# Optimization experiments

Hardware: AMD Instinct MI355X
Metric: run time of the kernel (lower is better)

The kernel has to match this reference:

```python
import jax, jax.numpy as jnp
import numpy as np

B, S, D = 4, 4096, 2048
H, HD = 16, 128
FFN = 8192
CAP = 0.25
TOP_K = int(S * CAP)  # 1024
EPS = 1e-6


def rmsnorm(x, g):
    return x * jax.lax.rsqrt(jnp.mean(x * x, axis=-1, keepdims=True) + EPS) * g


def apply_rope(x, cos, sin):
    # x: [b,t,h,hd]; cos/sin: [t, hd//2]
    half = x.shape[-1] // 2
    x1, x2 = x[..., :half], x[..., half:]
    c = cos[None, :, None, :]
    s = sin[None, :, None, :]
    return jnp.concatenate([x1 * c - x2 * s, x1 * s + x2 * c], axis=-1)


def transformer_block(x, mask, freqs_cis, g1, wq, wk, wv, wo, g2, w1, w3, w2):
    b, t, d = x.shape
    cos, sin = freqs_cis[..., 0], freqs_cis[..., 1]
    h = rmsnorm(x, g1)
    q = (h @ wq).reshape(b, t, H, HD)
    k = (h @ wk).reshape(b, t, H, HD)
    v = (h @ wv).reshape(b, t, H, HD)
    q = apply_rope(q, cos, sin)
    k = apply_rope(k, cos, sin)
    scores = jnp.einsum('bqhd,bkhd->bhqk', q, k) / np.sqrt(HD) + mask[None, None]
    attn = jax.nn.softmax(scores, axis=-1)
    o = jnp.einsum('bhqk,bkhd->bqhd', attn, v).reshape(b, t, d) @ wo
    x = x + o
    h2 = rmsnorm(x, g2)
    x = x + (jax.nn.silu(h2 @ w1) * (h2 @ w3)) @ w2
    return x, None


def setup_inputs() -> dict:
    key = jax.random.key(0)
    ks = jax.random.split(key, 12)
    w = lambda k, shp: jax.random.normal(k, shp, dtype=jnp.float32) * 0.02
    return {
        'x': jax.random.normal(ks[0], (B, S, D), dtype=jnp.float32),
        'mask': jnp.zeros((TOP_K, TOP_K), dtype=jnp.float32),
        'freqs_cis': jax.random.uniform(ks[1], (TOP_K, HD // 2, 2), dtype=jnp.float32),
        'w_router': w(ks[2], (D,)),
        'g1': jnp.ones((D,), dtype=jnp.float32),
        'wq': w(ks[3], (D, D)),
        'wk': w(ks[4], (D, D)),
        'wv': w(ks[5], (D, D)),
        'wo': w(ks[6], (D, D)),
        'g2': jnp.ones((D,), dtype=jnp.float32),
        'w1': w(ks[7], (D, FFN)),
        'w3': w(ks[8], (D, FFN)),
        'w2': w(ks[9], (FFN, D)),
    }


def reference(x, mask, freqs_cis, w_router, g1, wq, wk, wv, wo, g2, w1, w3, w2):
    b, s, d = x.shape
    # router: Linear(dim, 1, bias=False) -> [b, s]
    router_logits = jnp.einsum('bsd,d->bs', x, w_router)
    vals, idx = jax.lax.top_k(router_logits, TOP_K)  # [b, k]
    # sort selected indices ascending; permute weights to match (softmax is
    # permutation-equivariant so softmax-then-permute == torch's gather order)
    order = jnp.argsort(idx, axis=1)
    sel = jnp.take_along_axis(idx, order, axis=1)          # [b, k]
    w_sel = jnp.take_along_axis(vals, order, axis=1)       # [b, k]
    r_weights = jax.nn.softmax(w_sel, axis=1)[..., None]   # [b, k, 1]
    filtered_x = jnp.take_along_axis(x, sel[..., None], axis=1)  # [b, k, d]
    x_out, _ = transformer_block(filtered_x, mask, freqs_cis, g1, wq, wk, wv, wo, g2, w1, w3, w2)
    xw_out = r_weights * x_out
    b_idx = jnp.arange(b)[:, None]
    out = x.at[b_idx, sel].add(xw_out)
    return out
```

## Files before the change

### kernel.cpp

```cpp
#include <hip/hip_runtime.h>
#include <cstdint>
#include <cstddef>

#define NB 4
#define NS 4096
#define ND 2048
#define NH 16
#define NHD 128
#define NT 1024
#define NF 8192

typedef __bf16 bf16;
typedef __bf16 bf16x8 __attribute__((ext_vector_type(8)));
typedef __bf16 bf16x4 __attribute__((ext_vector_type(4)));
typedef float  f32x4  __attribute__((ext_vector_type(4)));

typedef const __attribute__((address_space(1))) void* gptr_t;
typedef __attribute__((address_space(3))) void* lptr_t;

__device__ __forceinline__ float wave_sum(float v) {
#pragma unroll
    for (int off = 32; off > 0; off >>= 1) v += __shfl_xor(v, off);
    return v;
}
__device__ __forceinline__ float wave_max(float v) {
#pragma unroll
    for (int off = 32; off > 0; off >>= 1) v = fmaxf(v, __shfl_xor(v, off));
    return v;
}

__global__ __launch_bounds__(256) void router_k(const float* __restrict__ x,
                                                const float* __restrict__ wr,
                                                float* __restrict__ logits) {
    __shared__ float r4[4];
    long long row = blockIdx.x;
    const float4* xr = (const float4*)(x + row * ND);
    const float4* w4 = (const float4*)wr;
    float p = 0.f;
    for (int i = threadIdx.x; i < ND / 4; i += 256) {
        float4 a = xr[i], b = w4[i];
        p += a.x * b.x + a.y * b.y + a.z * b.z + a.w * b.w;
    }
    p = wave_sum(p);
    if ((threadIdx.x & 63) == 0) r4[threadIdx.x >> 6] = p;
    __syncthreads();
    if (threadIdx.x == 0) logits[row] = r4[0] + r4[1] + r4[2] + r4[3];
}

__global__ __launch_bounds__(1024) void topk_k(const float* __restrict__ logits,
                                               int* __restrict__ sel,
                                               float* __restrict__ rw) {
    __shared__ unsigned long long keys[NS];
    __shared__ float r16[16];
    __shared__ float bmax, bsum;
    const int bb = blockIdx.x;
    const int tid = threadIdx.x;
    const float* lg = logits + (long long)bb * NS;

    for (int i = tid; i < NS; i += 1024) {
        unsigned u = __float_as_uint(lg[i]);
        u = (u & 0x80000000u) ? ~u : (u | 0x80000000u);
        keys[i] = ((unsigned long long)u << 32) | (unsigned)(NS - 1 - i);
    }
    __syncthreads();
    for (int k = 2; k <= NS; k <<= 1) {
        for (int j = k >> 1; j > 0; j >>= 1) {
            for (int i = tid; i < NS; i += 1024) {
                int ixj = i ^ j;
                if (ixj > i) {
                    unsigned long long a = keys[i], c = keys[ixj];
                    bool up = ((i & k) == 0);
                    if (up ? (a < c) : (a > c)) { keys[i] = c; keys[ixj] = a; }
                }
            }
            __syncthreads();
        }
    }
    unsigned long long a0 = keys[tid];
    __syncthreads();
    {
        unsigned idx_ = NS - 1 - (unsigned)(a0 & 0xFFFFFFFFu);
        unsigned uval = (unsigned)(a0 >> 32);
        keys[tid] = ((unsigned long long)idx_ << 32) | uval;
    }
    __syncthreads();
    for (int k = 2; k <= NT; k <<= 1) {
        for (int j = k >> 1; j > 0; j >>= 1) {
            int i = tid, ixj = i ^ j;
            if (i < NT && ixj > i) {
                unsigned long long a = keys[i], c = keys[ixj];
                bool up = ((i & k) == 0);
                if (up ? (a > c) : (a < c)) { keys[i] = c; keys[ixj] = a; }
            }
            __syncthreads();
        }
    }
    unsigned long long kk = keys[tid];
    int si = (int)(kk >> 32);
    unsigned u = (unsigned)(kk & 0xFFFFFFFFu);
    u = (u & 0x80000000u) ? (u ^ 0x80000000u) : ~u;
    float val = __uint_as_float(u);

    const int wid = tid >> 6, lane = tid & 63;
    float mx = wave_max(val);
    if (lane == 0) r16[wid] = mx;
    __syncthreads();
    if (tid == 0) {
        float m = r16[0];
        for (int i = 1; i < 16; i++) m = fmaxf(m, r16[i]);
        bmax = m;
    }
    __syncthreads();
    float e = __expf(val - bmax);
    float s = wave_sum(e);
    if (lane == 0) r16[wid] = s;
    __syncthreads();
    if (tid == 0) {
        float t = 0.f;
        for (int i = 0; i < 16; i++) t += r16[i];
        bsum = t;
    }
    __syncthreads();
    sel[bb * NT + tid] = si;
    rw[bb * NT + tid] = e / bsum;
}

__global__ __launch_bounds__(256) void gather_k(const float* __restrict__ x,
                                                const int* __restrict__ sel,
                                                float* __restrict__ xf) {
    int gid = blockIdx.x * 256 + threadIdx.x;
    int col = gid & (ND / 4 - 1);
    int row = gid >> 9;
    int bb = row >> 10;
    int s = sel[row];
    ((float4*)xf)[gid] = ((const float4*)x)[((long long)bb * NS + s) * (ND / 4) + col];
}

__global__ __launch_bounds__(256) void rmsnorm_k(const float* __restrict__ x,
                                                 const float* __restrict__ g,
                                                 bf16* __restrict__ out) {
    __shared__ float r4[4];
    __shared__ float scl;
    long long row = blockIdx.x;
    const float4* xr = (const float4*)(x + row * ND);
    int i0 = threadIdx.x, i1 = threadIdx.x + 256;
    float4 a = xr[i0], b = xr[i1];
    float ss = a.x * a.x + a.y * a.y + a.z * a.z + a.w * a.w +
               b.x * b.x + b.y * b.y + b.z * b.z + b.w * b.w;
    ss = wave_sum(ss);
    if ((threadIdx.x & 63) == 0) r4[threadIdx.x >> 6] = ss;
    __syncthreads();
    if (threadIdx.x == 0)
        scl = rsqrtf((r4[0] + r4[1] + r4[2] + r4[3]) * (1.0f / ND) + 1e-6f);
    __syncthreads();
    float s = scl;
    const float4* g4 = (const float4*)g;
    float4 ga = g4[i0], gb = g4[i1];
    bf16x4 o0, o1;
    o0[0] = (bf16)(a.x * s * ga.x); o0[1] = (bf16)(a.y * s * ga.y);
    o0[2] = (bf16)(a.z * s * ga.z); o0[3] = (bf16)(a.w * s * ga.w);
    o1[0] = (bf16)(b.x * s * gb.x); o1[1] = (bf16)(b.y * s * gb.y);
    o1[2] = (bf16)(b.z * s * gb.z); o1[3] = (bf16)(b.w * s * gb.w);
    *(bf16x4*)(out + row * ND + i0 * 4) = o0;
    *(bf16x4*)(out + row * ND + i1 * 4) = o1;
}

__global__ __launch_bounds__(256) void transpose_to_bf16(const float* __restrict__ in,
                                                         bf16* __restrict__ out,
                                                         int R, int C) {
    __shared__ float tile[32][33];
    int bx = blockIdx.x * 32;
    int by = blockIdx.y * 32;
    int tx = threadIdx.x & 31;
    int ty = threadIdx.x >> 5;
#pragma unroll
    for (int i = 0; i < 4; i++)
        tile[ty + 8 * i][tx] = in[(long long)(by + ty + 8 * i) * C + bx + tx];
    __syncthreads();
#pragma unroll
    for (int i = 0; i < 4; i++)
        out[(long long)(bx + ty + 8 * i) * R + by + tx] = (bf16)tile[tx][ty + 8 * i];
}

__global__ __launch_bounds__(256) void transpose4_nd(const float* __restrict__ s0,
                                                     const float* __restrict__ s1,
                                                     const float* __restrict__ s2,
                                                     const float* __restrict__ s3,
                                                     bf16* __restrict__ d_wqkv,
                                                     bf16* __restrict__ d_wo) {
    __shared__ float tile[32][33];
    const int z = blockIdx.z;
    const float* in = (z == 0) ? s0 : (z == 1) ? s1 : (z == 2) ? s2 : s3;
    bf16* out = (z < 3) ? (d_wqkv + (size_t)z * ND * ND) : d_wo;
    int bx = blockIdx.x * 32;
    int by = blockIdx.y * 32;
    int tx = threadIdx.x & 31;
    int ty = threadIdx.x >> 5;
#pragma unroll
    for (int i = 0; i < 4; i++)
        tile[ty + 8 * i][tx] = in[(long long)(by + ty + 8 * i) * ND + bx + tx];
    __syncthreads();
#pragma unroll
    for (int i = 0; i < 4; i++)
        out[(long long)(bx + ty + 8 * i) * ND + by + tx] = (bf16)tile[tx][ty + 8 * i];
}

__global__ __launch_bounds__(256) void transpose2_ff(const float* __restrict__ s0,
                                                     const float* __restrict__ s1,
                                                     bf16* __restrict__ dst) {
    __shared__ float tile[32][33];
    const int z = blockIdx.z;
    const float* in = z ? s1 : s0;
    bf16* out = dst + (size_t)z * ND * NF;
    int bx = blockIdx.x * 32;
    int by = blockIdx.y * 32;
    int tx = threadIdx.x & 31;
    int ty = threadIdx.x >> 5;
#pragma unroll
    for (int i = 0; i < 4; i++)
        tile[ty + 8 * i][tx] = in[(long long)(by + ty + 8 * i) * NF + bx + tx];
    __syncthreads();
#pragma unroll
    for (int i = 0; i < 4; i++)
        out[(long long)(bx + ty + 8 * i) * ND + by + tx] = (bf16)tile[tx][ty + 8 * i];
}

__global__ __launch_bounds__(256) void rope_qk_k(const bf16* __restrict__ QKV,
                                                 const float* __restrict__ fr,
                                                 bf16* __restrict__ Q,
                                                 bf16* __restrict__ K) {
    int gid = blockIdx.x * 256 + threadIdx.x;
    int hd = gid & 63;
    int h = (gid >> 6) & 15;
    int t = (gid >> 10) & (NT - 1);
    int bb = gid >> 20;
    float c = fr[t * 128 + hd * 2 + 0];
    float s = fr[t * 128 + hd * 2 + 1];
    long long base = ((long long)bb * NT + t) * (3 * ND) + h * NHD;
    float q1 = (float)QKV[base + hd],      q2 = (float)QKV[base + hd + 64];
    float k1 = (float)QKV[base + ND + hd], k2 = (float)QKV[base + ND + hd + 64];
    long long ob = (((long long)(bb * NH + h)) * NT + t) * NHD;
    Q[ob + hd]      = (bf16)(q1 * c - q2 * s);
    Q[ob + hd + 64] = (bf16)(q1 * s + q2 * c);
    K[ob + hd]      = (bf16)(k1 * c - k2 * s);
    K[ob + hd + 64] = (bf16)(k1 * s + k2 * c);
}

__global__ __launch_bounds__(256) void vtr_k(const bf16* __restrict__ QKV,
                                             bf16* __restrict__ Vt) {
    __shared__ bf16 tile[64][136];
    const int tt = blockIdx.x * 64;
    const int bh = blockIdx.y;
    const int bb = bh >> 4, h = bh & 15;
    const int tid = threadIdx.x;

    const int lt = tid >> 4;
    const int ld = (tid & 15) * 8;
#pragma unroll
    for (int i = 0; i < 4; i++) {
        int t = i * 16 + lt;
        bf16x8 v = *(const bf16x8*)(QKV + ((size_t)(bb * NT) + tt + t) * (3 * ND)
                                    + 2 * ND + h * NHD + ld);
        *(bf16x8*)&tile[t][ld] = v;
    }
    __syncthreads();

    const int d = tid >> 1;
    const int j0 = (tid & 1) * 32;
    bf16 tmp[32];
#pragma unroll
    for (int j = 0; j < 32; j++) tmp[j] = tile[j0 + j][d];
    bf16* dst = Vt + ((size_t)bh * NHD + d) * NT + tt + j0;
#pragma unroll
    for (int j = 0; j < 4; j++)
        *(bf16x8*)(dst + j * 8) = *(const bf16x8*)(tmp + j * 8);
}

__global__ __launch_bounds__(256) void copy_k(const float4* __restrict__ in,
                                              float4* __restrict__ out, long long n) {
    for (long long i = (long long)blockIdx.x * 256 + threadIdx.x; i < n;
         i += (long long)gridDim.x * 256)
        out[i] = in[i];
}

__global__ __launch_bounds__(256, 2) void flash_k(
    const bf16* __restrict__ Qr,
    const bf16* __restrict__ Kr,
    const bf16* __restrict__ Vt,
    bf16* __restrict__ O) {
    __shared__ char lds[81920];

    const int tid = threadIdx.x;
    const int lane = tid & 63;
    const int w = tid >> 6;
    const int lm = lane & 15, lq = lane >> 4;
    const int lm7 = lm & 7;

    const int bh = blockIdx.y;
    const int q0 = blockIdx.x * 128;
    const bf16* Qb = Qr + (size_t)bh * NT * NHD;
    const bf16* Kb = Kr + (size_t)bh * NT * NHD;
    const bf16* Vb = Vt + (size_t)bh * NHD * NT;

    const int krow = tid >> 4;
    const int kc_s = (tid & 15);
    const int vrow = tid >> 3;
    const int vc_s = (tid & 7);

    bf16x8 q[2][4];
#pragma unroll
    for (int mi = 0; mi < 2; mi++)
#pragma unroll
        for (int ks = 0; ks < 4; ks++)
            q[mi][ks] = *(const bf16x8*)(Qb + (size_t)(q0 + w * 32 + mi * 16 + lm) * NHD
                                         + lq * 8 + ks * 32);

    f32x4 o0[8], o1[8];
#pragma unroll
    for (int i = 0; i < 8; i++) {
        f32x4 zz = {0.f, 0.f, 0.f, 0.f};
        o0[i] = zz; o1[i] = zz;
    }
    float m0[4], m1[4], l0[4], l1[4];
#pragma unroll
    for (int r = 0; r < 4; r++) {
        m0[r] = -3.0e38f; m1[r] = -3.0e38f; l0[r] = 0.f; l1[r] = 0.f;
    }

    char* Pb = lds + 65536 + w * 4096;
    const float kscal = 0.08838834764831845f * 1.4426950408889634f;

#pragma unroll
    for (int i = 0; i < 4; i++) {
        int row = i * 16 + krow;
        __builtin_amdgcn_global_load_lds(
            (gptr_t)(Kb + (size_t)row * NHD + (kc_s ^ (row & 7)) * 8),
            (lptr_t)(lds + i * 4096 + tid * 16), 16, 0, 0);
    }
#pragma unroll
    for (int i = 0; i < 4; i++) {
        int row = i * 32 + vrow;
        __builtin_amdgcn_global_load_lds(
            (gptr_t)(Vb + (size_t)row * NT + (vc_s ^ (row & 7)) * 8),
            (lptr_t)(lds + 32768 + i * 4096 + tid * 16), 16, 0, 0);
    }
    __syncthreads();

    for (int c = 0; c < 16; ++c) {
        char* Kl = lds + (c & 1) * 16384;
        char* Vl = lds + 32768 + (c & 1) * 16384;

        if (c < 15) {
            const int key1 = (c + 1) * 64;
            char* Kd = lds + ((c + 1) & 1) * 16384;
            char* Vd = lds + 32768 + ((c + 1) & 1) * 16384;
#pragma unroll
            for (int i = 0; i < 4; i++) {
                int row = i * 16 + krow;
                __builtin_amdgcn_global_load_lds(
                    (gptr_t)(Kb + (size_t)(key1 + row) * NHD + (kc_s ^ (row & 7)) * 8),
                    (lptr_t)(Kd + i * 4096 + tid * 16), 16, 0, 0);
            }
#pragma unroll
            for (int i = 0; i < 4; i++) {
                int row = i * 32 + vrow;
                __builtin_amdgcn_global_load_lds(
                    (gptr_t)(Vb + (size_t)row * NT + key1 + (vc_s ^ (row & 7)) * 8),
                    (lptr_t)(Vd + i * 4096 + tid * 16), 16, 0, 0);
            }
        }

        f32x4 s0[4], s1[4];
#pragma unroll
        for (int ni = 0; ni < 4; ni++) {
            f32x4 zz = {0.f, 0.f, 0.f, 0.f};
            s0[ni] = zz; s1[ni] = zz;
        }
        __builtin_amdgcn_s_setprio(1);
#pragma unroll
        for (int ni = 0; ni < 4; ni++) {
#pragma unroll
            for (int ks = 0; ks < 4; ks++) {
                bf16x8 kf = *(const bf16x8*)(Kl + (lm + 16 * ni) * 256
                                             + (((lq + 4 * ks) ^ lm7) << 4));
                s0[ni] = __builtin_amdgcn_mfma_f32_16x16x32_bf16(q[0][ks], kf, s0[ni], 0, 0, 0);
                s1[ni] = __builtin_amdgcn_mfma_f32_16x16x32_bf16(q[1][ks], kf, s1[ni], 0, 0, 0);
            }
        }
        __builtin_amdgcn_s_setprio(0);

#pragma unroll
        for (int ni = 0; ni < 4; ni++)
#pragma unroll
            for (int r = 0; r < 4; r++) {
                s0[ni][r] *= kscal;
                s1[ni][r] *= kscal;
            }

        float sc0[4], sc1[4];
#pragma unroll
        for (int r = 0; r < 4; r++) {
            float a0 = fmaxf(fmaxf(s0[0][r], s0[1][r]), fmaxf(s0[2][r], s0[3][r]));
            float a1 = fmaxf(fmaxf(s1[0][r], s1[1][r]), fmaxf(s1[2][r], s1[3][r]));
#pragma unroll
            for (int o = 1; o < 16; o <<= 1) {
                a0 = fmaxf(a0, __shfl_xor(a0, o));
                a1 = fmaxf(a1, __shfl_xor(a1, o));
            }
            float mn0 = fmaxf(m0[r], a0);
            float mn1 = fmaxf(m1[r], a1);
            sc0[r] = exp2f(m0[r] - mn0);
            sc1[r] = exp2f(m1[r] - mn1);
            m0[r] = mn0; m1[r] = mn1;

            float rs0 = 0.f, rs1 = 0.f;
#pragma unroll
            for (int ni = 0; ni < 4; ni++) {
                float p0 = exp2f(s0[ni][r] - mn0);
                float p1 = exp2f(s1[ni][r] - mn1);
                s0[ni][r] = p0; s1[ni][r] = p1;
                rs0 += p0; rs1 += p1;
            }
#pragma unroll
            for (int o = 1; o < 16; o <<= 1) {
                rs0 += __shfl_xor(rs0, o);
                rs1 += __shfl_xor(rs1, o);
            }
            l0[r] = l0[r] * sc0[r] + rs0;
            l1[r] = l1[r] * sc1[r] + rs1;
        }
#pragma unroll
        for (int ni = 0; ni < 8; ni++)
#pragma unroll
            for (int r = 0; r < 4; r++) {
                o0[ni][r] *= sc0[r];
                o1[ni][r] *= sc1[r];
            }

#pragma unroll
        for (int ni = 0; ni < 4; ni++)
#pragma unroll
            for (int r = 0; r < 4; r++) {
                int q_l0 = lq * 4 + r;
                int q_l1 = 16 + q_l0;
                int cw = (lm >> 3) + 2 * ni;
                *(bf16*)(Pb + q_l0 * 128 + ((cw ^ (q_l0 & 7)) << 4) + (lm7 << 1)) =
                    (bf16)s0[ni][r];
                *(bf16*)(Pb + q_l1 * 128 + ((cw ^ (q_l1 & 7)) << 4) + (lm7 << 1)) =
                    (bf16)s1[ni][r];
            }
        asm volatile("s_waitcnt lgkmcnt(0)" ::: "memory");
        __builtin_amdgcn_sched_barrier(0);

        __builtin_amdgcn_s_setprio(1);
#pragma unroll
        for (int ks = 0; ks < 2; ks++) {
            bf16x8 pa0 = *(const bf16x8*)(Pb + lm * 128 + (((lq + 4 * ks) ^ lm7) << 4));
            bf16x8 pa1 = *(const bf16x8*)(Pb + (lm + 16) * 128 + (((lq + 4 * ks) ^ lm7) << 4));
#pragma unroll
            for (int ni = 0; ni < 8; ni++) {
                bf16x8 vf = *(const bf16x8*)(Vl + (lm + 16 * ni) * 128
                                             + (((lq + 4 * ks) ^ lm7) << 4));
                o0[ni] = __builtin_amdgcn_mfma_f32_16x16x32_bf16(pa0, vf, o0[ni], 0, 0, 0);
                o1[ni] = __builtin_amdgcn_mfma_f32_16x16x32_bf16(pa1, vf, o1[ni], 0, 0, 0);
            }
        }
        __builtin_amdgcn_s_setprio(0);

        __syncthreads();
    }

    const int bb = bh >> 4, h = bh & 15;
    float rl0[4], rl1[4];
#pragma unroll
    for (int r = 0; r < 4; r++) { rl0[r] = 1.f / l0[r]; rl1[r] = 1.f / l1[r]; }
#pragma unroll
    for (int ni = 0; ni < 8; ni++) {
#pragma unroll
        for (int r = 0; r < 4; r++) {
            int col = h * 128 + lm + 16 * ni;
            long long r0 = (long long)bb * NT + q0 + w * 32 + lq * 4 + r;
            O[(r0) * ND + col]      = (bf16)(o0[ni][r] * rl0[r]);
            O[(r0 + 16) * ND + col] = (bf16)(o1[ni][r] * rl1[r]);
        }
    }
}

#define G256_SB() __builtin_amdgcn_sched_barrier(0)
#define G256_LGKM(n) do { asm volatile("s_waitcnt lgkmcnt(" #n ")" ::: "memory"); \
    __builtin_amdgcn_sched_barrier(0); } while (0)
#define G256_VMC(n) do { asm volatile("s_waitcnt vmcnt(" #n ")" ::: "memory"); \
    __builtin_amdgcn_sched_barrier(0); } while (0)

#define MFMA_Q(mlo, nlo) do { \
    __builtin_amdgcn_s_setprio(1); \
    _Pragma("unroll") \
    for (int _ks = 0; _ks < 2; _ks++) \
    _Pragma("unroll") \
    for (int _mi = 0; _mi < 4; _mi++) \
    _Pragma("unroll") \
    for (int _ni = 0; _ni < 2; _ni++) \
        acc[(mlo) + _mi][(nlo) + _ni] = __builtin_amdgcn_mfma_f32_16x16x32_bf16( \
            a[(mlo) + _mi][_ks], b[(nlo) + _ni][_ks], acc[(mlo) + _mi][(nlo) + _ni], \
            0, 0, 0); \
    __builtin_amdgcn_s_setprio(0); \
} while (0)

template <int MODE>
__global__ __launch_bounds__(512, 2) void gemm256(
    const bf16* __restrict__ A, int lda,
    const bf16* __restrict__ Bt, int ldb,
    void* __restrict__ Cv, int ldc,
    int K, float alpha,
    const bf16* __restrict__ Bt2,
    const float* __restrict__ res, const int* __restrict__ selp,
    const float* __restrict__ rwp, float* __restrict__ outp) {

    constexpr bool DUALB = (MODE == 6);
    constexpr bool N128  = (MODE == 2 || MODE == 5 || MODE == 7);
    constexpr bool NI4   = !N128;
    constexpr int  BBUF  = N128 ? 16384 : 32768;
    constexpr int  BUFS  = 32768 + BBUF;
    constexpr int  bStep2 = DUALB ? 16384 : 4096;
    __shared__ char smem[2 * BUFS];

    const int tid = threadIdx.x;
    const int lane = tid & 63;
    const int wid = tid >> 6;
    const int wm = N128 ? (wid >> 1) : (wid >> 2);
    const int wn = N128 ? (wid & 1) : (wid & 3);
    const int lm = lane & 15, lq = lane >> 4;

    const int nx = gridDim.x;
    const int orig = blockIdx.y * nx + blockIdx.x;
    const int xcd = orig & 7;
    const int r_ = orig >> 3;
    const int mi_ = r_ & 7, ni_ = r_ >> 3;
    const int nT = (DUALB || N128) ? 128 : 256;
    const int m0 = ((xcd >> 2) * 8 + mi_) * 256;
    const int n0 = ((xcd & 3) * (nx >> 2) + ni_) * nT;
    const long long kz = (long long)blockIdx.z * K;

    const int srow = tid >> 3;
    const int skc = ((tid & 7) ^ (srow & 7)) * 8;
    const long long stA = (long long)64 * lda;
    const long long stB = (long long)64 * ldb;
    const bf16* gA = A + (long long)(m0 + srow) * lda + kz + skc;
    const bf16* gB0 = Bt + (long long)(n0 + srow) * ldb + kz + skc;
    const bf16* gB2 = DUALB ? Bt2 + (long long)(n0 + srow) * ldb + kz + skc
                            : gB0 + 2 * stB;

    char* sm = (char*)smem;
    const int sdst = tid * 16;

    auto stage = [&](int c, int t) {
        char* lA = sm + c * BUFS + sdst;
        long long ko = (long long)t * 64;
#pragma unroll
        for (int i = 0; i < 4; i++)
            __builtin_amdgcn_global_load_lds((gptr_t)(gA + i * stA + ko),
                                             (lptr_t)(lA + i * 8192), 16, 0, 0);
        char* lB = sm + c * BUFS + 32768 + sdst;
        __builtin_amdgcn_global_load_lds((gptr_t)(gB0 + ko), (lptr_t)lB, 16, 0, 0);
        __builtin_amdgcn_global_load_lds((gptr_t)(gB0 + stB + ko),
                                         (lptr_t)(lB + 8192), 16, 0, 0);
        if constexpr (NI4) {
            __builtin_amdgcn_global_load_lds((gptr_t)(gB2 + ko),
                                             (lptr_t)(lB + 16384), 16, 0, 0);
            __builtin_amdgcn_global_load_lds((gptr_t)(gB2 + stB + ko),
                                             (lptr_t)(lB + 24576), 16, 0, 0);
        }
    };

    const int swz = (lq ^ (lm & 7)) << 4;
    const int aoff = ((N128 ? wm * 64 : wm * 128) + lm) * 128 + swz;
    const int boff = ((N128 ? wn * 64 : (DUALB ? wn * 32 : wn * 64)) + lm) * 128 + swz;

    f32x4 acc[8][4];
#pragma unroll
    for (int i = 0; i < 8; i++)
#pragma unroll
        for (int j = 0; j < 4; j++) {
            f32x4 zz = {0.f, 0.f, 0.f, 0.f};
            acc[i][j] = zz;
        }
    bf16x8 a[8][2], b[4][2];

    auto ldA4 = [&](char* bA, int lo) {
#pragma unroll
        for (int mi2 = 0; mi2 < 4; mi2++) {
            a[lo + mi2][0] = *(const bf16x8*)(bA + aoff + (lo + mi2) * 2048);
            a[lo + mi2][1] = *(const bf16x8*)(bA + (aoff ^ 64) + (lo + mi2) * 2048);
        }
    };
    auto ldB2 = [&](char* bB, int lo) {
#pragma unroll
        for (int ni2 = 0; ni2 < 2; ni2++) {
            int ix = lo + ni2;
            int o;
            if constexpr (N128)
                o = boff + ix * 2048;
            else
                o = boff + (ix & 1) * 2048 + (ix >> 1) * bStep2;
            b[ix][0] = *(const bf16x8*)(bB + o);
            b[ix][1] = *(const bf16x8*)(bB + (o ^ 64));
        }
    };

    const int NTk = K >> 6;

    stage(0, 0);
    stage(1, 1);
    if constexpr (NI4) { G256_VMC(8); } else { G256_VMC(6); }
    __builtin_amdgcn_s_barrier();
    G256_SB();

    for (int t = 0; t < NTk; ++t) {
        const int c = t & 1;
        char* bA = sm + c * BUFS;
        char* bB = bA + 32768;

        if constexpr (N128) {
            ldA4(bA, 0);
            ldB2(bB, 0);
            G256_SB();
            ldB2(bB, 2);
            G256_SB();

            G256_LGKM(4);
            MFMA_Q(0, 0);
            G256_LGKM(0);
            __builtin_amdgcn_s_barrier();
            G256_SB();
            const bool more = (t + 2 < NTk);
            if (more) stage(c, t + 2);
            G256_SB();
            MFMA_Q(0, 2);
            if (more) { G256_VMC(6); } else { G256_VMC(0); }
            __builtin_amdgcn_s_barrier();
            G256_SB();
        } else {
            ldA4(bA, 0);
            ldB2(bB, 0);
            G256_SB();
            ldB2(bB, 2);
            G256_SB();
            ldA4(bA, 4);
            G256_SB();

            G256_LGKM(12);
            MFMA_Q(0, 0);
            G256_LGKM(8);
            MFMA_Q(0, 2);
            G256_LGKM(0);
            __builtin_amdgcn_s_barrier();
            G256_SB();
            const bool more = (t + 2 < NTk);
            if (more) stage(c, t + 2);
            G256_SB();
            MFMA_Q(4, 0);
            MFMA_Q(4, 2);
            if (more) { G256_VMC(8); } else { G256_VMC(0); }
            __builtin_amdgcn_s_barrier();
            G256_SB();
        }
    }

    if constexpr (MODE == 6) {
        bf16* C = (bf16*)Cv;
#pragma unroll
        for (int mi = 0; mi < 8; mi++) {
#pragma unroll
            for (int ni = 0; ni < 2; ni++) {
                const int row = m0 + wm * 128 + mi * 16 + lq * 4;
                const int col = n0 + wn * 32 + ni * 16 + lm;
#pragma unroll
                for (int r = 0; r < 4; r++) {
                    float v1 = acc[mi][ni][r];
                    float v3 = acc[mi][ni + 2][r];
                    C[(long long)(row + r) * ldc + col] =
                        (bf16)((v1 / (1.f + __expf(-v1))) * v3);
                }
            }
        }
    } else {
#pragma unroll
        for (int mi = 0; mi < 4; mi++) {
#pragma unroll
            for (int ni = 0; ni < 4; ni++) {
                const int row = m0 + wm * 64 + mi * 16 + lq * 4;
                const int col = n0 + wn * 64 + ni * 16 + lm;
#pragma unroll
                for (int r = 0; r < 4; r++) {
                    float v = alpha * acc[mi][ni][r];
                    long long rr = row + r;
                    if constexpr (MODE == 7) {
                        bf16* C = (bf16*)Cv;
                        C[rr * ldc + col] = (bf16)v;
                    } else if constexpr (MODE == 2) {
                        float* C = (float*)Cv;
                        C[rr * ldc + col] += v;
                    } else {
                        int bb2 = (int)(rr >> 10);
                        int s = selp[rr];
                        float add = rwp[rr] * (v + res[rr * (long long)ND + col]);
                        outp[((long long)bb2 * NS + s) * ND + col] += add;
                    }
                }
            }
        }
    }
}

extern "C" void kernel_launch(void* const* d_in, const int* in_sizes, int n_in,
                              void* d_out, int out_size, void* d_ws, size_t ws_size,
                              hipStream_t stream) {
    const float* x  = (const float*)d_in[0];
    const float* fr = (const float*)d_in[2];
    const float* wr = (const float*)d_in[3];
    const float* g1 = (const float*)d_in[4];
    const float* wq = (const float*)d_in[5];
    const float* wk = (const float*)d_in[6];
    const float* wv = (const float*)d_in[7];
    const float* wo = (const float*)d_in[8];
    const float* g2 = (const float*)d_in[9];
    const float* w1 = (const float*)d_in[10];
    const float* w3 = (const float*)d_in[11];
    const float* w2 = (const float*)d_in[12];
    float* out = (float*)d_out;

    char* ws = (char*)d_ws;
    size_t off = 0;
    auto take = [&](size_t bytes) -> char* {
        char* p = ws + off;
        off += (bytes + 255) & ~(size_t)255;
        return p;
    };
    int*   sel    = (int*)take((size_t)NB * NT * 4);
    float* rw     = (float*)take((size_t)NB * NT * 4);
    float* logits = (float*)take((size_t)NB * NS * 4);
    float* xf     = (float*)take((size_t)NB * NT * ND * 4);
    bf16*  hbuf   = (bf16*)take((size_t)NB * NT * ND * 2);
    bf16*  wqkv_t = (bf16*)take((size_t)3 * ND * ND * 2);
    bf16*  wo_t   = (bf16*)take((size_t)ND * ND * 2);
    bf16*  Obuf   = (bf16*)take((size_t)NB * NT * ND * 2);
    char* xr = ws + off;
    bf16* QKV = (bf16*)xr;
    bf16* Qr  = QKV + (size_t)NB * NT * 3 * ND;
    bf16* Kr  = Qr + (size_t)NB * NT * ND;
    bf16* Vt  = Kr + (size_t)NB * NT * ND;
    bf16* w1_t  = (bf16*)xr;
    bf16* w3_t  = w1_t + (size_t)ND * NF;
    bf16* w2_t  = w3_t + (size_t)ND * NF;
    bf16* inter = w2_t + (size_t)ND * NF;

    router_k<<<NB * NS, 256, 0, stream>>>(x, wr, logits);
    topk_k<<<NB, 1024, 0, stream>>>(logits, sel, rw);
    gather_k<<<(NB * NT * ND / 4) / 256, 256, 0, stream>>>(x, sel, xf);
    rmsnorm_k<<<NB * NT, 256, 0, stream>>>(xf, g1, hbuf);

    transpose4_nd<<<dim3(ND / 32, ND / 32, 4), 256, 0, stream>>>(
        wq, wk, wv, wo, wqkv_t, wo_t);

    gemm256<7><<<dim3(3 * ND / 128, NB * NT / 256, 1), 512, 0, stream>>>(
        hbuf, ND, wqkv_t, ND, QKV, 3 * ND, ND, 1.0f,
        nullptr, nullptr, nullptr, nullptr, nullptr);

    rope_qk_k<<<(NB * NT * NH * 64) / 256, 256, 0, stream>>>(QKV, fr, Qr, Kr);
    vtr_k<<<dim3(NT / 64, NB * NH), 256, 0, stream>>>(QKV, Vt);

    flash_k<<<dim3(NT / 128, NB * NH), 256, 0, stream>>>(Qr, Kr, Vt, Obuf);

    gemm256<2><<<dim3(ND / 128, NB * NT / 256, 1), 512, 0, stream>>>(
        Obuf, ND, wo_t, ND, xf, ND, ND, 1.0f,
        nullptr, nullptr, nullptr, nullptr, nullptr);

    rmsnorm_k<<<NB * NT, 256, 0, stream>>>(xf, g2, hbuf);

    transpose2_ff<<<dim3(NF / 32, ND / 32, 2), 256, 0, stream>>>(w1, w3, w1_t);
    transpose_to_bf16<<<dim3(ND / 32, NF / 32), 256, 0, stream>>>(w2, w2_t, NF, ND);

    gemm256<6><<<dim3(NF / 128, NB * NT / 256, 1), 512, 0, stream>>>(
        hbuf, ND, w1_t, ND, inter, NF, ND, 1.0f,
        w3_t, nullptr, nullptr, nullptr, nullptr);

    copy_k<<<8192, 256, 0, stream>>>((const float4*)x, (float4*)out,
                                     (long long)NB * NS * ND / 4);
    gemm256<5><<<dim3(ND / 128, NB * NT / 256, 1), 512, 0, stream>>>(
        inter, NF, w2_t, NF, nullptr, ND, NF, 1.0f,
        nullptr, xf, sel, rw, out);
}
```

Before: 1.249 ms.

## Load B fragments directly from global into registers in dual-B GEMM

For the dual-weight (w1/w3) GEMM mode, B tiles are no longer staged through LDS. Each wave now loads its own B fragments straight from global memory into registers, prefetched one k-step ahead, while A stays double-buffered in LDS. The goal is to cut LDS traffic and shared-memory footprint so more blocks fit per CU. The trade-off is uncoalesced direct global loads, higher register pressure from the prefetch buffer, and loss of B reuse across waves. The non-N128 single-B path is removed, so only the dual-B and N128 modes remain supported.

```diff
diff --git a/kernel.cpp b/kernel.cpp
--- a/kernel.cpp
+++ b/kernel.cpp
@@ -518,10 +518,7 @@
 
     constexpr bool DUALB = (MODE == 6);
     constexpr bool N128  = (MODE == 2 || MODE == 5 || MODE == 7);
-    constexpr bool NI4   = !N128;
-    constexpr int  BBUF  = N128 ? 16384 : 32768;
-    constexpr int  BUFS  = 32768 + BBUF;
-    constexpr int  bStep2 = DUALB ? 16384 : 4096;
+    constexpr int  BUFS  = DUALB ? 32768 : 49152;
     __shared__ char smem[2 * BUFS];
 
     const int tid = threadIdx.x;
@@ -536,9 +533,8 @@
     const int xcd = orig & 7;
     const int r_ = orig >> 3;
     const int mi_ = r_ & 7, ni_ = r_ >> 3;
-    const int nT = (DUALB || N128) ? 128 : 256;
     const int m0 = ((xcd >> 2) * 8 + mi_) * 256;
-    const int n0 = ((xcd & 3) * (nx >> 2) + ni_) * nT;
+    const int n0 = ((xcd & 3) * (nx >> 2) + ni_) * 128;
     const long long kz = (long long)blockIdx.z * K;
 
     const int srow = tid >> 3;
@@ -547,34 +543,34 @@
     const long long stB = (long long)64 * ldb;
     const bf16* gA = A + (long long)(m0 + srow) * lda + kz + skc;
     const bf16* gB0 = Bt + (long long)(n0 + srow) * ldb + kz + skc;
-    const bf16* gB2 = DUALB ? Bt2 + (long long)(n0 + srow) * ldb + kz + skc
-                            : gB0 + 2 * stB;
 
     char* sm = (char*)smem;
     const int sdst = tid * 16;
 
-    auto stage = [&](int c, int t) {
+    auto stageA = [&](int c, int t) {
         char* lA = sm + c * BUFS + sdst;
         long long ko = (long long)t * 64;
 #pragma unroll
         for (int i = 0; i < 4; i++)
             __builtin_amdgcn_global_load_lds((gptr_t)(gA + i * stA + ko),
                                              (lptr_t)(lA + i * 8192), 16, 0, 0);
+    };
+    auto stageB_n128 = [&](int c, int t) {
         char* lB = sm + c * BUFS + 32768 + sdst;
+        long long ko = (long long)t * 64;
         __builtin_amdgcn_global_load_lds((gptr_t)(gB0 + ko), (lptr_t)lB, 16, 0, 0);
         __builtin_amdgcn_global_load_lds((gptr_t)(gB0 + stB + ko),
                                          (lptr_t)(lB + 8192), 16, 0, 0);
-        if constexpr (NI4) {
-            __builtin_amdgcn_global_load_lds((gptr_t)(gB2 + ko),
-                                             (lptr_t)(lB + 16384), 16, 0, 0);
-            __builtin_amdgcn_global_load_lds((gptr_t)(gB2 + stB + ko),
-                                             (lptr_t)(lB + 24576), 16, 0, 0);
-        }
     };
 
     const int swz = (lq ^ (lm & 7)) << 4;
     const int aoff = ((N128 ? wm * 64 : wm * 128) + lm) * 128 + swz;
-    const int boff = ((N128 ? wn * 64 : (DUALB ? wn * 32 : wn * 64)) + lm) * 128 + swz;
+    const int boff = ((N128 ? wn * 64 : 0) + lm) * 128 + swz;
+
+    const bf16* bp0 = Bt  + (long long)(n0 + (DUALB ? wn * 32 : 0) + lm) * ldb + kz + lq * 8;
+    const bf16* bp1 = bp0 + (long long)16 * ldb;
+    const bf16* bp2 = (DUALB ? Bt2 : Bt) + (long long)(n0 + (DUALB ? wn * 32 : 0) + lm) * ldb + kz + lq * 8;
+    const bf16* bp3 = bp2 + (long long)16 * ldb;
 
     f32x4 acc[8][4];
 #pragma unroll
@@ -584,7 +580,18 @@
             f32x4 zz = {0.f, 0.f, 0.f, 0.f};
             acc[i][j] = zz;
         }
-    bf16x8 a[8][2], b[4][2];
+    bf16x8 a[8][2], b[4][2], bnx[4][2];
+
+    auto loadBdir = [&](int t) {
+        long long ko = (long long)t * 64;
+#pragma unroll
+        for (int ks = 0; ks < 2; ks++) {
+            bnx[0][ks] = *(const bf16x8*)(bp0 + ko + ks * 32);
+            bnx[1][ks] = *(const bf16x8*)(bp1 + ko + ks * 32);
+            bnx[2][ks] = *(const bf16x8*)(bp2 + ko + ks * 32);
+            bnx[3][ks] = *(const bf16x8*)(bp3 + ko + ks * 32);
+        }
+    };
 
     auto ldA4 = [&](char* bA, int lo) {
 #pragma unroll
@@ -593,15 +600,11 @@
             a[lo + mi2][1] = *(const bf16x8*)(bA + (aoff ^ 64) + (lo + mi2) * 2048);
         }
     };
-    auto ldB2 = [&](char* bB, int lo) {
+    auto ldB2_n128 = [&](char* bB, int lo) {
 #pragma unroll
         for (int ni2 = 0; ni2 < 2; ni2++) {
             int ix = lo + ni2;
-            int o;
-            if constexpr (N128)
-                o = boff + ix * 2048;
-            else
-                o = boff + (ix & 1) * 2048 + (ix >> 1) * bStep2;
+            int o = boff + ix * 2048;
             b[ix][0] = *(const bf16x8*)(bB + o);
             b[ix][1] = *(const bf16x8*)(bB + (o ^ 64));
         }
@@ -609,22 +612,69 @@
 
     const int NTk = K >> 6;
 
-    stage(0, 0);
-    stage(1, 1);
-    if constexpr (NI4) { G256_VMC(8); } else { G256_VMC(6); }
-    __builtin_amdgcn_s_barrier();
-    G256_SB();
-
-    for (int t = 0; t < NTk; ++t) {
-        const int c = t & 1;
-        char* bA = sm + c * BUFS;
-        char* bB = bA + 32768;
-
-        if constexpr (N128) {
+    if constexpr (DUALB) {
+        stageA(0, 0);
+        loadBdir(0);
+        stageA(1, 1);
+        G256_VMC(4);
+#pragma unroll
+        for (int ix = 0; ix < 4; ix++) {
+            b[ix][0] = bnx[ix][0]; b[ix][1] = bnx[ix][1];
+        }
+        __builtin_amdgcn_s_barrier();
+        G256_SB();
+
+        for (int t = 0; t < NTk; ++t) {
+            const int c = t & 1;
+            char* bA = sm + c * BUFS;
+            const bool more1 = (t + 1 < NTk);
+            const bool more2 = (t + 2 < NTk);
+
+            if (more1) loadBdir(t + 1);
+            G256_SB();
             ldA4(bA, 0);
-            ldB2(bB, 0);
-            G256_SB();
-            ldB2(bB, 2);
+            G256_SB();
+            ldA4(bA, 4);
+            G256_SB();
+
+            G256_LGKM(8);
+            MFMA_Q(0, 0);
+            MFMA_Q(0, 2);
+            G256_LGKM(0);
+            __builtin_amdgcn_s_barrier();
+            G256_SB();
+            if (more2) stageA(c, t + 2);
+            G256_SB();
+            MFMA_Q(4, 0);
+            MFMA_Q(4, 2);
+            if (more2) { G256_VMC(12); }
+            else if (more1) { G256_VMC(8); }
+            else { G256_VMC(0); }
+            __builtin_amdgcn_s_barrier();
+            G256_SB();
+            if (more1) {
+#pragma unroll
+                for (int ix = 0; ix < 4; ix++) {
+                    b[ix][0] = bnx[ix][0]; b[ix][1] = bnx[ix][1];
+                }
+            }
+        }
+    } else {
+        stageA(0, 0); stageB_n128(0, 0);
+        stageA(1, 1); stageB_n128(1, 1);
+        G256_VMC(6);
+        __builtin_amdgcn_s_barrier();
+        G256_SB();
+
+        for (int t = 0; t < NTk; ++t) {
+            const int c = t & 1;
+            char* bA = sm + c * BUFS;
+            char* bB = bA + 32768;
+
+            ldA4(bA, 0);
+            ldB2_n128(bB, 0);
+            G256_SB();
+            ldB2_n128(bB, 2);
             G256_SB();
 
             G256_LGKM(4);
@@ -633,34 +683,10 @@
             __builtin_amdgcn_s_barrier();
             G256_SB();
             const bool more = (t + 2 < NTk);
-            if (more) stage(c, t + 2);
+            if (more) { stageA(c, t + 2); stageB_n128(c, t + 2); }
             G256_SB();
             MFMA_Q(0, 2);
             if (more) { G256_VMC(6); } else { G256_VMC(0); }
-            __builtin_amdgcn_s_barrier();
-            G256_SB();
-        } else {
-            ldA4(bA, 0);
-            ldB2(bB, 0);
-            G256_SB();
-            ldB2(bB, 2);
-            G256_SB();
-            ldA4(bA, 4);
-            G256_SB();
-
-            G256_LGKM(12);
-            MFMA_Q(0, 0);
-            G256_LGKM(8);
-            MFMA_Q(0, 2);
-            G256_LGKM(0);
-            __builtin_amdgcn_s_barrier();
-            G256_SB();
-            const bool more = (t + 2 < NTk);
-            if (more) stage(c, t + 2);
-            G256_SB();
-            MFMA_Q(4, 0);
-            MFMA_Q(4, 2);
-            if (more) { G256_VMC(8); } else { G256_VMC(0); }
             __builtin_amdgcn_s_barrier();
             G256_SB();
         }
```

Result: slower. 1.626 ms (+30.2%).
